# Optimization experiments

Hardware: AMD Instinct MI355X
Metric: run time of the kernel (lower is better)

The kernel has to match this reference:

```python
import jax, jax.numpy as jnp
import numpy as np

EPS = 1e-3  # Keras BatchNormalization default epsilon


def _conv2d_same(x, w):
    # x: [N,H,W,Cin], w: [kh,kw,Cin,Cout]
    return jax.lax.conv_general_dilated(
        x, w, window_strides=(1, 1), padding='SAME',
        dimension_numbers=('NHWC', 'HWIO', 'NHWC'))


def _hard_sigmoid(x):
    return jnp.clip(0.2 * x + 0.5, 0.0, 1.0)


def _convlstm2d(x, Wx, Wh, b):
    # x: [B,T,H,W,Cin]; Wx: [3,3,Cin,4F]; Wh: [3,3,F,4F]; b: [4F]
    B, T, H, W, Cin = x.shape
    F = Wh.shape[2]
    # precompute input-to-gate convs for all timesteps at once
    xg = _conv2d_same(x.reshape(B * T, H, W, Cin), Wx).reshape(B, T, H, W, 4 * F) + b

    def step(carry, xt):
        h, c = carry
        g = xt + _conv2d_same(h, Wh)
        gi, gf, gc, go = jnp.split(g, 4, axis=-1)  # Keras gate order i,f,c,o
        i = _hard_sigmoid(gi)
        f = _hard_sigmoid(gf)
        o = _hard_sigmoid(go)
        c = f * c + i * jnp.tanh(gc)
        h = o * jnp.tanh(c)
        return (h, c), h

    h0 = jnp.zeros((B, H, W, F), x.dtype)
    (_, _), hs = jax.lax.scan(step, (h0, h0), jnp.moveaxis(xg, 1, 0))
    return jnp.moveaxis(hs, 0, 1)  # [B,T,H,W,F]


def _batchnorm(x, g, be, m, v):
    # inference-mode BN over channel axis
    return (x - m) * (g * jax.lax.rsqrt(v + EPS)) + be


def setup_inputs() -> dict:
    key = jax.random.key(0)
    ks = jax.random.split(key, 10)
    B, T, H, W, C, F, NC = 16, 64, 16, 16, 6, 96, 10
    s = 0.05
    x = jax.random.normal(ks[0], (B, T, H, W, C), jnp.float32)
    Wx0 = jax.random.normal(ks[1], (3, 3, C, 4 * F), jnp.float32) * s
    Wh0 = jax.random.normal(ks[2], (3, 3, F, 4 * F), jnp.float32) * s
    b0 = jnp.zeros((4 * F,), jnp.float32)
    g0 = jnp.ones((F,), jnp.float32)
    be0 = jnp.zeros((F,), jnp.float32)
    m0 = jax.random.normal(ks[3], (F,), jnp.float32) * 0.1
    v0 = jax.random.uniform(ks[4], (F,), jnp.float32) + 0.5
    Wx1 = jax.random.normal(ks[5], (3, 3, F, 4 * F), jnp.float32) * s
    Wh1 = jax.random.normal(ks[6], (3, 3, F, 4 * F), jnp.float32) * s
    b1 = jnp.zeros((4 * F,), jnp.float32)
    g1 = jnp.ones((F,), jnp.float32)
    be1 = jnp.zeros((F,), jnp.float32)
    m1 = jax.random.normal(ks[7], (F,), jnp.float32) * 0.1
    v1 = jax.random.uniform(ks[8], (F,), jnp.float32) + 0.5
    Wd = jax.random.normal(ks[9], (T * H * W * F, NC), jnp.float32) * 0.001
    bd = jnp.zeros((NC,), jnp.float32)
    return dict(x=x, Wx0=Wx0, Wh0=Wh0, b0=b0, g0=g0, be0=be0, m0=m0, v0=v0,
                Wx1=Wx1, Wh1=Wh1, b1=b1, g1=g1, be1=be1, m1=m1, v1=v1,
                Wd=Wd, bd=bd)


def reference(x, Wx0, Wh0, b0, g0, be0, m0, v0,
              Wx1, Wh1, b1, g1, be1, m1, v1, Wd, bd):
    h = _convlstm2d(x, Wx0, Wh0, b0)
    h = _batchnorm(h, g0, be0, m0, v0)
    h = _convlstm2d(h, Wx1, Wh1, b1)
    h = _batchnorm(h, g1, be1, m1, v1)
    B = h.shape[0]
    flat = h.reshape(B, -1)  # Keras Flatten (row-major, channels-last)
    return flat @ Wd + bd
```

## Files before the change

kernel.cpp:

```cpp
#include <hip/hip_runtime.h>
#include <math.h>


typedef __attribute__((ext_vector_type(8))) short     bf16x8;
typedef __attribute__((ext_vector_type(8))) unsigned short u16x8;
typedef __attribute__((ext_vector_type(4))) float     f32x4;
typedef unsigned short u16;

#define RS 393216

__device__ __forceinline__ float hsig(float x) {
    return fminf(fmaxf(0.2f * x + 0.5f, 0.0f), 1.0f);
}
__device__ __forceinline__ float bf2f(u16 u) {
    union { unsigned int i; float f; } v; v.i = ((unsigned int)u) << 16; return v.f;
}
__device__ __forceinline__ u16 f2bf(float f) {
    union { float f; unsigned int i; } v; v.f = f;
    unsigned int r = (v.i + 0x7FFFu + ((v.i >> 16) & 1u)) >> 16;
    return (u16)r;
}

__device__ __forceinline__ void gridbar(unsigned* ctrs, unsigned* epoch,
                                        unsigned k, int blk)
{
    __syncthreads();
    if (threadIdx.x == 0) {
        __builtin_amdgcn_fence(__ATOMIC_RELEASE, "agent");
        __hip_atomic_fetch_add(ctrs + (blk & 63) * 64, 1u,
                               __ATOMIC_RELAXED, __HIP_MEMORY_SCOPE_AGENT);
    }
    if (blk == 0 && threadIdx.x < 64) {
        const unsigned target = k * 256u;
        unsigned sum;
        do {
            unsigned v = __hip_atomic_load(ctrs + threadIdx.x * 64,
                                           __ATOMIC_RELAXED,
                                           __HIP_MEMORY_SCOPE_AGENT);
            sum = v;
#pragma unroll
            for (int m = 1; m < 64; m <<= 1)
                sum += __shfl_xor(sum, m, 64);
            if (sum < target) __builtin_amdgcn_s_sleep(2);
        } while (sum < target);
        if (threadIdx.x == 0)
            __hip_atomic_store(epoch, k, __ATOMIC_RELAXED,
                               __HIP_MEMORY_SCOPE_AGENT);
    }
    if (threadIdx.x == 0) {
        while (__hip_atomic_load(epoch, __ATOMIC_RELAXED,
                                 __HIP_MEMORY_SCOPE_AGENT) < k)
            __builtin_amdgcn_s_sleep(4);
        __builtin_amdgcn_fence(__ATOMIC_ACQUIRE, "agent");
    }
    __syncthreads();
}

__device__ __forceinline__ void xbar(unsigned* slots, int myslot,
                                     unsigned target)
{
    __syncthreads();
    if (threadIdx.x == 0)
        __hip_atomic_fetch_add(slots + myslot * 32, 1u,
                               __ATOMIC_RELAXED, __HIP_MEMORY_SCOPE_AGENT);
    if (threadIdx.x < 32) {
        unsigned sum;
        do {
            unsigned v = __hip_atomic_load(slots + threadIdx.x * 32,
                                           __ATOMIC_RELAXED,
                                           __HIP_MEMORY_SCOPE_AGENT);
            sum = v;
#pragma unroll
            for (int m = 1; m < 32; m <<= 1)
                sum += __shfl_xor(sum, m, 64);
            if (sum < target) __builtin_amdgcn_s_sleep(2);
        } while (sum < target);
        asm volatile("buffer_inv sc0\n\ts_waitcnt vmcnt(0)" ::: "memory");
    }
    __syncthreads();
}

__global__ __launch_bounds__(256) void prep_x(const float* __restrict__ x,
                                              u16* __restrict__ xpad)
{
    const int idx = blockIdx.x * 256 + threadIdx.x;
    const int t = idx >> 12, b = (idx >> 8) & 15, p = idx & 255;
    const float* src = x + (((size_t)b * 64 + t) * 256 + p) * 6;
    u16x8 v = {};
    v[0] = f2bf(src[0]); v[1] = f2bf(src[1]); v[2] = f2bf(src[2]);
    v[3] = f2bf(src[3]); v[4] = f2bf(src[4]); v[5] = f2bf(src[5]);
    *(u16x8*)(xpad + (size_t)idx * 8) = v;
}

__global__ __launch_bounds__(256) void wtrans0(const float* __restrict__ Wx0,
                                               const float* __restrict__ Wh0,
                                               u16* __restrict__ Wt0)
{
    const int idx = blockIdx.x * 256 + threadIdx.x;
    const int n = idx / 960, k = idx - n * 960;
    const int nt = n / 96, j = n - nt * 96;
    const int no = (j / 24) * 96 + nt * 24 + (j % 24);
    float v = 0.0f;
    if (k < 96) {
        const int q = k >> 3, c = k & 7;
        if (q < 9 && c < 6) v = Wx0[(q * 6 + c) * 384 + no];
    } else {
        v = Wh0[(k - 96) * 384 + no];
    }
    Wt0[idx] = f2bf(v);
}

__global__ __launch_bounds__(256) void wtrans1(const float* __restrict__ Wx1,
                                               const float* __restrict__ Wh1,
                                               u16* __restrict__ Wt1)
{
    const int idx = blockIdx.x * 256 + threadIdx.x;
    const int n = idx / 1728, k = idx - n * 1728;
    const int nt = n / 96, j = n - nt * 96;
    const int no = (j / 24) * 96 + nt * 24 + (j % 24);
    const float v = (k < 864) ? Wx1[k * 384 + no] : Wh1[(k - 864) * 384 + no];
    Wt1[idx] = f2bf(v);
}

__global__ __launch_bounds__(256) void wtransD(const float* __restrict__ Wd,
                                               u16* __restrict__ WdT)
{
    const int k = blockIdx.x * 256 + threadIdx.x;
    const float* src = Wd + (size_t)k * 10;
#pragma unroll
    for (int nc = 0; nc < 10; ++nc)
        WdT[(size_t)nc * 1572864 + k] = f2bf(src[nc]);
}

__device__ void phase(int t, int m0, int n0, int tidx, char* lds,
    const u16* __restrict__ xpad, u16* __restrict__ h0b,
    u16* __restrict__ h1b, u16* __restrict__ h0bnb, u16* __restrict__ hall,
    const u16* __restrict__ Wt0, const u16* __restrict__ Wt1,
    const float* __restrict__ b0, const float* __restrict__ b1,
    const float* __restrict__ g0, const float* __restrict__ be0,
    const float* __restrict__ mu0, const float* __restrict__ v0,
    const float* __restrict__ g1, const float* __restrict__ be1,
    const float* __restrict__ mu1, const float* __restrict__ v1,
    float (&cregs)[6])
{
    const int half = tidx >> 8;
    const int htid = tidx & 255;
    const bool active = half ? (t < 63) : (t >= 0);

    const u16* in0 = half ? (xpad + (size_t)(t + 1) * 32768)
                          : (h0bnb + (size_t)(t & 1) * RS);
    const u16* in1 = half ? (h0b + (size_t)(t & 1) * RS)
                          : (h1b + (size_t)((t - 1) & 1) * RS);
    u16* hraw_out = half ? (h0b + (size_t)((t + 1) & 1) * RS)
                         : (h1b + (size_t)(t & 1) * RS);
    u16* hbn_out  = half ? (h0bnb + (size_t)((t + 1) & 1) * RS)
                         : (hall + (size_t)(t < 0 ? 0 : t) * RS);

    const int lane = htid & 63;
    const int hw   = htid >> 6;
    const int wm = hw >> 1, wn = hw & 1;
    const int fr = lane & 15, fg = lane >> 4;
    const int arow = htid >> 2, seg = htid & 3;
    const int mg = m0 + arow;
    const int py = (mg >> 4) & 15, px = mg & 15, pb = mg >> 8;
    const int nt = n0 / 96;

    const int   KT   = half ? 960 : 1728;
    const int   NS0  = half ? 3   : 27;
    const int   MYST = half ? 30  : 54;
    const u16*  Wt   = half ? Wt0 : Wt1;

    u16*   AsB  = (u16*)(lds + half * 25600);
    u16*   BsB  = AsB + 5120;
    float* accS = (float*)(lds + half * 25600);

    f32x4 acc[2][3];
#pragma unroll
    for (int i = 0; i < 2; ++i)
#pragma unroll
        for (int j = 0; j < 3; ++j) acc[i][j] = (f32x4){0.f, 0.f, 0.f, 0.f};

    u16x8 va, vb0, vb1;
    auto stage = [&](int ks) {
        u16x8 z = {};
        va = z;
        if (half && ks < 3) {
            const int q = ks * 4 + seg;
            const int qd = q / 3;
            const int yy = py + qd - 1;
            const int xx = px + (q - 3 * qd) - 1;
            if (q < 9 && (unsigned)yy < 16u && (unsigned)xx < 16u)
                va = *(const u16x8*)(in0 + (size_t)((pb << 8) + yy * 16 + xx) * 8);
        } else {
            const int s = (ks < NS0) ? ks : ks - NS0;
            const u16* src = (ks < NS0) ? in0 : in1;
            const int q = s / 3;
            const int c0v = (s - 3 * q) * 32 + seg * 8;
            const int qd = q / 3;
            const int yy = py + qd - 1;
            const int xx = px + (q - 3 * qd) - 1;
            if ((unsigned)yy < 16u && (unsigned)xx < 16u)
                va = *(const u16x8*)(src + (size_t)((pb << 8) + yy * 16 + xx) * 96 + c0v);
        }
        const int koff = ks * 32 + seg * 8;
        vb0 = *(const u16x8*)(Wt + (size_t)(n0 + arow) * KT + koff);
        vb1 = z;
        if (htid < 128)
            vb1 = *(const u16x8*)(Wt + (size_t)(n0 + 64 + arow) * KT + koff);
    };
    auto ldsw = [&](int buf) {
        *(u16x8*)(AsB + buf * 2560 + arow * 40 + seg * 8) = va;
        *(u16x8*)(BsB + buf * 3840 + arow * 40 + seg * 8) = vb0;
        if (htid < 128)
            *(u16x8*)(BsB + buf * 3840 + (64 + arow) * 40 + seg * 8) = vb1;
    };

    if (active) { stage(0); ldsw(0); }
    __syncthreads();

    for (int ks = 0; ks < 54; ++ks) {
        const int cur = ks & 1;
        if (active && ks < MYST) {
            if (ks + 1 < MYST) stage(ks + 1);

            bf16x8 af[2], bq[3];
#pragma unroll
            for (int mf = 0; mf < 2; ++mf)
                af[mf] = *(const bf16x8*)(AsB + cur * 2560 +
                                          (wm * 32 + mf * 16 + fr) * 40 + fg * 8);
#pragma unroll
            for (int nf = 0; nf < 3; ++nf)
                bq[nf] = *(const bf16x8*)(BsB + cur * 3840 +
                                          (wn * 48 + nf * 16 + fr) * 40 + fg * 8);

            __builtin_amdgcn_s_setprio(1);
#pragma unroll
            for (int mf = 0; mf < 2; ++mf)
#pragma unroll
                for (int nf = 0; nf < 3; ++nf)
                    acc[mf][nf] = __builtin_amdgcn_mfma_f32_16x16x32_bf16(
                        af[mf], bq[nf], acc[mf][nf], 0, 0, 0);
            __builtin_amdgcn_s_setprio(0);

            if (ks + 1 < MYST) ldsw(cur ^ 1);
        }
        __syncthreads();
    }

    if (active) {
        const float* bias = half ? b0 : b1;
#pragma unroll
        for (int nf = 0; nf < 3; ++nf) {
            const int col = wn * 48 + nf * 16 + fr;
            const float bi = bias[(col / 24) * 96 + nt * 24 + (col % 24)];
#pragma unroll
            for (int mf = 0; mf < 2; ++mf) {
                const int row = wm * 32 + mf * 16 + fg * 4;
#pragma unroll
                for (int r = 0; r < 4; ++r)
                    accS[(row + r) * 100 + col] = acc[mf][nf][r] + bi;
            }
        }
    }
    __syncthreads();

    if (active) {
        const float* gam = half ? g0 : g1;
        const float* bet = half ? be0 : be1;
        const float* muv = half ? mu0 : mu1;
        const float* var = half ? v0  : v1;
#pragma unroll
        for (int q = 0; q < 6; ++q) {
            const int item = htid + 256 * q;
            const int r = item / 24, fl = item - r * 24;
            const float gi = accS[r * 100 + fl];
            const float gf = accS[r * 100 + 24 + fl];
            const float gc = accS[r * 100 + 48 + fl];
            const float go = accS[r * 100 + 72 + fl];
            const int f = nt * 24 + fl;
            const float i_ = hsig(gi);
            const float f_ = hsig(gf);
            const float o_ = hsig(go);
            const float c_ = f_ * cregs[q] + i_ * tanhf(gc);
            const float h_ = o_ * tanhf(c_);
            cregs[q] = c_;
            hraw_out[(size_t)(m0 + r) * 96 + f] = f2bf(h_);
            const float s = gam[f] * rsqrtf(var[f] + 1e-3f);
            hbn_out[(size_t)(m0 + r) * 96 + f] =
                f2bf((h_ - muv[f]) * s + bet[f]);
        }
    }
}

__global__ __launch_bounds__(512, 2) void fused(
    unsigned* bctrs, unsigned* bepoch, unsigned* reg8, unsigned* xslots,
    const u16* xpad, u16* h0b, u16* h1b, u16* h0bnb, u16* hall,
    const u16* Wt0, const u16* Wt1,
    const float* b0, const float* b1,
    const float* g0, const float* be0, const float* mu0, const float* v0,
    const float* g1, const float* be1, const float* mu1, const float* v1)
{
    __shared__ char lds[51200];
    __shared__ unsigned shinfo[3];
    const int blk = blockIdx.x;

    if (threadIdx.x == 0) {
        unsigned xcc;
        asm volatile("s_getreg_b32 %0, hwreg(HW_REG_XCC_ID)" : "=s"(xcc));
        xcc &= 7u;
        unsigned slot = __hip_atomic_fetch_add(reg8 + xcc * 64, 1u,
                                               __ATOMIC_RELAXED,
                                               __HIP_MEMORY_SCOPE_AGENT);
        shinfo[0] = xcc; shinfo[1] = slot;
    }
    gridbar(bctrs, bepoch, 1, blk);
    if (threadIdx.x == 0) {
        unsigned ok = 1;
#pragma unroll
        for (int k = 0; k < 8; ++k)
            ok &= (__hip_atomic_load(reg8 + k * 64, __ATOMIC_RELAXED,
                                     __HIP_MEMORY_SCOPE_AGENT) == 32u);
        shinfo[2] = ok;
    }
    __syncthreads();
    const unsigned grp  = shinfo[0];
    const unsigned slot = shinfo[1];
    const bool grouped  = (shinfo[2] != 0u);

    float cregs[6] = {0.f, 0.f, 0.f, 0.f, 0.f, 0.f};

    if (grouped) {
        const int m0 = (int)grp * 512 + (int)(slot >> 2) * 64;
        const int n0 = (int)(slot & 3) * 96;
        unsigned* gs = xslots + grp * 1024;
        unsigned bar = 0;
        for (int t = -1; t < 64; ++t) {
            phase(t, m0, n0, threadIdx.x, lds, xpad, h0b, h1b, h0bnb, hall,
                  Wt0, Wt1, b0, b1, g0, be0, mu0, v0, g1, be1, mu1, v1, cregs);
            xbar(gs, (int)slot, (++bar) * 32u);
        }
    } else {
        const int m0 = (blk >> 2) * 64;
        const int n0 = (blk & 3) * 96;
        unsigned bar = 1;
        for (int t = -1; t < 64; ++t) {
            phase(t, m0, n0, threadIdx.x, lds, xpad, h0b, h1b, h0bnb, hall,
                  Wt0, Wt1, b0, b1, g0, be0, mu0, v0, g1, be1, mu1, v1, cregs);
            gridbar(bctrs, bepoch, ++bar, blk);
        }
    }
}

__global__ __launch_bounds__(512, 2) void stepF(int t,
    const u16* xpad, u16* h0b, u16* h1b, u16* h0bnb, u16* hall,
    const u16* Wt0, const u16* Wt1,
    const float* b0, const float* b1,
    const float* g0, const float* be0, const float* mu0, const float* v0,
    const float* g1, const float* be1, const float* mu1, const float* v1,
    float* c0g, float* c1g)
{
    __shared__ char lds[51200];
    const int m0 = (blockIdx.x >> 2) * 64;
    const int n0 = (blockIdx.x & 3) * 96;
    const int half = threadIdx.x >> 8;
    const int htid = threadIdx.x & 255;
    const int nt = n0 / 96;
    float* cst = half ? c0g : c1g;

    float cregs[6];
#pragma unroll
    for (int q = 0; q < 6; ++q) {
        const int item = htid + 256 * q;
        const int r = item / 24, fl = item - r * 24;
        cregs[q] = cst[(size_t)(m0 + r) * 96 + nt * 24 + fl];
    }
    phase(t, m0, n0, threadIdx.x, lds, xpad, h0b, h1b, h0bnb, hall,
          Wt0, Wt1, b0, b1, g0, be0, mu0, v0, g1, be1, mu1, v1, cregs);
#pragma unroll
    for (int q = 0; q < 6; ++q) {
        const int item = htid + 256 * q;
        const int r = item / 24, fl = item - r * 24;
        cst[(size_t)(m0 + r) * 96 + nt * 24 + fl] = cregs[q];
    }
}

__global__ void dense_partial(const u16* __restrict__ hall,
                              const u16* __restrict__ WdT,
                              float* __restrict__ partial)
{
    const int k0 = blockIdx.x * 2048;
    const int tt = k0 / 24576;
    const int r0 = k0 - tt * 24576;
    const int th = threadIdx.x;
    const int b  = th / 10;
    const int nc = th - b * 10;
    const u16* hp = hall + (size_t)(tt * 16 + b) * 24576 + r0;
    const u16* wp = WdT + (size_t)nc * 1572864 + k0;
    float acc = 0.0f;
    for (int j = 0; j < 2048; j += 8) {
        const u16x8 hv = *(const u16x8*)(hp + j);
        const u16x8 wv = *(const u16x8*)(wp + j);
#pragma unroll
        for (int u = 0; u < 8; ++u)
            acc = fmaf(bf2f(hv[u]), bf2f(wv[u]), acc);
    }
    partial[blockIdx.x * 160 + th] = acc;
}

__global__ void dense_reduce(const float* __restrict__ partial,
                             const float* __restrict__ bd,
                             float* __restrict__ out)
{
    const int t = threadIdx.x;
    const int nc = t - (t / 10) * 10;
    float acc = bd[nc];
    for (int p = 0; p < 768; ++p) acc += partial[p * 160 + t];
    out[t] = acc;
}

extern "C" void kernel_launch(void* const* d_in, const int* in_sizes, int n_in,
                              void* d_out, int out_size, void* d_ws, size_t ws_size,
                              hipStream_t stream)
{
    const float* x    = (const float*)d_in[0];
    const float* Wx0  = (const float*)d_in[1];
    const float* Wh0  = (const float*)d_in[2];
    const float* b0p  = (const float*)d_in[3];
    const float* g0p  = (const float*)d_in[4];
    const float* be0p = (const float*)d_in[5];
    const float* mu0p = (const float*)d_in[6];
    const float* v0p  = (const float*)d_in[7];
    const float* Wx1  = (const float*)d_in[8];
    const float* Wh1  = (const float*)d_in[9];
    const float* b1p  = (const float*)d_in[10];
    const float* g1p  = (const float*)d_in[11];
    const float* be1p = (const float*)d_in[12];
    const float* mu1p = (const float*)d_in[13];
    const float* v1p  = (const float*)d_in[14];
    const float* Wd   = (const float*)d_in[15];
    const float* bd   = (const float*)d_in[16];
    float* out = (float*)d_out;

    char* base = (char*)d_ws;
    u16*   h0b    = (u16*)(base);
    u16*   h1b    = (u16*)(base + 1572864);
    u16*   h0bnb  = (u16*)(base + 3145728);
    float* c0g    = (float*)(base + 4718592);
    float* c1g    = (float*)(base + 6291456);
    u16*   xpad   = (u16*)(base + 7864320);
    u16*   Wt0    = (u16*)(base + 12058624);
    u16*   Wt1    = (u16*)(base + 12795904);
    u16*   hall   = (u16*)(base + 14123008);
    float* part   = (float*)(base + 64454656);
    u16*   WdT    = (u16*)(base + 64946176);
    unsigned* bctrs  = (unsigned*)(base + 96403456);
    unsigned* bepoch = (unsigned*)(base + 96419840);
    unsigned* reg8   = (unsigned*)(base + 96420096);
    unsigned* xslots = (unsigned*)(base + 96422144);

    hipMemsetAsync(base, 0, 7864320, stream);
    hipMemsetAsync(bctrs, 0, 51456, stream);

    prep_x <<<1024, 256, 0, stream>>>(x, xpad);
    wtrans0<<<1440, 256, 0, stream>>>(Wx0, Wh0, Wt0);
    wtrans1<<<2592, 256, 0, stream>>>(Wx1, Wh1, Wt1);
    wtransD<<<6144, 256, 0, stream>>>(Wd, WdT);

    void* args[] = {
        (void*)&bctrs, (void*)&bepoch, (void*)&reg8, (void*)&xslots,
        (void*)&xpad, (void*)&h0b, (void*)&h1b, (void*)&h0bnb, (void*)&hall,
        (void*)&Wt0, (void*)&Wt1, (void*)&b0p, (void*)&b1p,
        (void*)&g0p, (void*)&be0p, (void*)&mu0p, (void*)&v0p,
        (void*)&g1p, (void*)&be1p, (void*)&mu1p, (void*)&v1p
    };
    hipError_t ce = hipLaunchCooperativeKernel((void*)fused, dim3(256),
                                               dim3(512), args, 0, stream);
    if (ce != hipSuccess) {
        (void)hipGetLastError();
        for (int t = -1; t < 64; ++t) {
            stepF<<<256, 512, 0, stream>>>(t, xpad, h0b, h1b, h0bnb, hall,
                                           Wt0, Wt1, b0p, b1p,
                                           g0p, be0p, mu0p, v0p,
                                           g1p, be1p, mu1p, v1p, c0g, c1g);
        }
    }

    dense_partial<<<768, 160, 0, stream>>>(hall, WdT, part);
    dense_reduce <<<1, 160, 0, stream>>>(part, bd, out);
}
```

Measured before the change: 1.975 ms.

## Load A fragments directly from global into registers, skipping LDS staging

The im2col A operand is now gathered straight from global memory into per-lane MFMA fragment registers, with two register sets (even/odd) prefetched two k-steps ahead, instead of being staged through LDS. Only the weight (B) tile still goes through double-buffered LDS, now with a row stride of 36 instead of 40. This removes the A-side LDS writes and reads and cuts LDS footprint. In exchange each lane issues scattered global loads, and duplicated A rows across waves are no longer shared, so global or cache traffic may rise.

```diff
diff --git a/kernel.cpp b/kernel.cpp
--- a/kernel.cpp
+++ b/kernel.cpp
@@ -19,6 +19,12 @@
     union { float f; unsigned int i; } v; v.f = f;
     unsigned int r = (v.i + 0x7FFFu + ((v.i >> 16) & 1u)) >> 16;
     return (u16)r;
+}
+__device__ __forceinline__ bf16x8 zsel(int4 v, bool ok) {
+    union { int4 i; bf16x8 b; } u;
+    u.i.x = ok ? v.x : 0; u.i.y = ok ? v.y : 0;
+    u.i.z = ok ? v.z : 0; u.i.w = ok ? v.w : 0;
+    return u.b;
 }
 
 __device__ __forceinline__ void gridbar(unsigned* ctrs, unsigned* epoch,
@@ -161,8 +167,7 @@
     const int wm = hw >> 1, wn = hw & 1;
     const int fr = lane & 15, fg = lane >> 4;
     const int arow = htid >> 2, seg = htid & 3;
-    const int mg = m0 + arow;
-    const int py = (mg >> 4) & 15, px = mg & 15, pb = mg >> 8;
+    const int pb = m0 >> 8;
     const int nt = n0 / 96;
 
     const int   KT   = half ? 960 : 1728;
@@ -170,8 +175,7 @@
     const int   MYST = half ? 30  : 54;
     const u16*  Wt   = half ? Wt0 : Wt1;
 
-    u16*   AsB  = (u16*)(lds + half * 25600);
-    u16*   BsB  = AsB + 5120;
+    u16*   BsB  = (u16*)(lds + half * 25600);
     float* accS = (float*)(lds + half * 25600);
 
     f32x4 acc[2][3];
@@ -180,70 +184,99 @@
 #pragma unroll
         for (int j = 0; j < 3; ++j) acc[i][j] = (f32x4){0.f, 0.f, 0.f, 0.f};
 
-    u16x8 va, vb0, vb1;
-    auto stage = [&](int ks) {
-        u16x8 z = {};
-        va = z;
-        if (half && ks < 3) {
-            const int q = ks * 4 + seg;
-            const int qd = q / 3;
-            const int yy = py + qd - 1;
-            const int xx = px + (q - 3 * qd) - 1;
-            if (q < 9 && (unsigned)yy < 16u && (unsigned)xx < 16u)
-                va = *(const u16x8*)(in0 + (size_t)((pb << 8) + yy * 16 + xx) * 8);
-        } else {
-            const int s = (ks < NS0) ? ks : ks - NS0;
-            const u16* src = (ks < NS0) ? in0 : in1;
-            const int q = s / 3;
-            const int c0v = (s - 3 * q) * 32 + seg * 8;
-            const int qd = q / 3;
-            const int yy = py + qd - 1;
-            const int xx = px + (q - 3 * qd) - 1;
-            if ((unsigned)yy < 16u && (unsigned)xx < 16u)
-                va = *(const u16x8*)(src + (size_t)((pb << 8) + yy * 16 + xx) * 96 + c0v);
+    int yf[2];
+#pragma unroll
+    for (int mf = 0; mf < 2; ++mf)
+        yf[mf] = ((m0 + wm * 32 + mf * 16) >> 4) & 15;
+
+    auto loadA = [&](int ks, bf16x8 (&af)[2]) {
+#pragma unroll
+        for (int mf = 0; mf < 2; ++mf) {
+            if (half && ks < 3) {
+                const int q  = ks * 4 + fg;
+                const int qd = q / 3;
+                const int qx = q - 3 * qd;
+                const int yy = yf[mf] + qd - 1;
+                const int xx = fr + qx - 1;
+                const bool ok = (q < 9) & ((unsigned)yy < 16u) &
+                                ((unsigned)xx < 16u);
+                const int yyc = yy < 0 ? 0 : (yy > 15 ? 15 : yy);
+                const int xxc = xx < 0 ? 0 : (xx > 15 ? 15 : xx);
+                const int4 v = *(const int4*)(in0 +
+                    (size_t)((pb << 8) + yyc * 16 + xxc) * 8);
+                af[mf] = zsel(v, ok);
+            } else {
+                const int s = (ks < NS0) ? ks : ks - NS0;
+                const u16* src = (ks < NS0) ? in0 : in1;
+                const int q  = s / 3;
+                const int c0 = (s - 3 * q) * 32 + fg * 8;
+                const int qd = q / 3;
+                const int qx = q - 3 * qd;
+                const int yy = yf[mf] + qd - 1;
+                if ((unsigned)yy < 16u) {
+                    const int xx = fr + qx - 1;
+                    const int xxc = xx < 0 ? 0 : (xx > 15 ? 15 : xx);
+                    const int4 v = *(const int4*)(src +
+                        (size_t)((pb << 8) + yy * 16 + xxc) * 96 + c0);
+                    af[mf] = zsel(v, (unsigned)xx < 16u);
+                } else {
+                    const bf16x8 z = {};
+                    af[mf] = z;
+                }
+            }
         }
+    };
+
+    u16x8 vb0, vb1;
+    auto stageB = [&](int ks) {
         const int koff = ks * 32 + seg * 8;
         vb0 = *(const u16x8*)(Wt + (size_t)(n0 + arow) * KT + koff);
-        vb1 = z;
         if (htid < 128)
             vb1 = *(const u16x8*)(Wt + (size_t)(n0 + 64 + arow) * KT + koff);
     };
-    auto ldsw = [&](int buf) {
-        *(u16x8*)(AsB + buf * 2560 + arow * 40 + seg * 8) = va;
-        *(u16x8*)(BsB + buf * 3840 + arow * 40 + seg * 8) = vb0;
+    auto writeB = [&](int buf) {
+        *(u16x8*)(BsB + buf * 3456 + arow * 36 + seg * 8) = vb0;
         if (htid < 128)
-            *(u16x8*)(BsB + buf * 3840 + (64 + arow) * 40 + seg * 8) = vb1;
+            *(u16x8*)(BsB + buf * 3456 + (64 + arow) * 36 + seg * 8) = vb1;
     };
 
-    if (active) { stage(0); ldsw(0); }
-    __syncthreads();
-
-    for (int ks = 0; ks < 54; ++ks) {
-        const int cur = ks & 1;
-        if (active && ks < MYST) {
-            if (ks + 1 < MYST) stage(ks + 1);
-
-            bf16x8 af[2], bq[3];
-#pragma unroll
-            for (int mf = 0; mf < 2; ++mf)
-                af[mf] = *(const bf16x8*)(AsB + cur * 2560 +
-                                          (wm * 32 + mf * 16 + fr) * 40 + fg * 8);
+    bf16x8 afe[2], afo[2];
+
+    if (active) {
+        loadA(0, afe);
+        loadA(1, afo);
+        stageB(0);
+        writeB(0);
+    }
+    __syncthreads();
+
+    auto step = [&](int ks, bf16x8 (&af)[2]) {
+        if (ks + 1 < MYST) stageB(ks + 1);
+
+        bf16x8 bq[3];
+#pragma unroll
+        for (int nf = 0; nf < 3; ++nf)
+            bq[nf] = *(const bf16x8*)(BsB + (ks & 1) * 3456 +
+                                      (wn * 48 + nf * 16 + fr) * 36 + fg * 8);
+
+        __builtin_amdgcn_s_setprio(1);
+#pragma unroll
+        for (int mf = 0; mf < 2; ++mf)
 #pragma unroll
             for (int nf = 0; nf < 3; ++nf)
-                bq[nf] = *(const bf16x8*)(BsB + cur * 3840 +
-                                          (wn * 48 + nf * 16 + fr) * 40 + fg * 8);
-
-            __builtin_amdgcn_s_setprio(1);
-#pragma unroll
-            for (int mf = 0; mf < 2; ++mf)
-#pragma unroll
-                for (int nf = 0; nf < 3; ++nf)
-                    acc[mf][nf] = __builtin_amdgcn_mfma_f32_16x16x32_bf16(
-                        af[mf], bq[nf], acc[mf][nf], 0, 0, 0);
-            __builtin_amdgcn_s_setprio(0);
-
-            if (ks + 1 < MYST) ldsw(cur ^ 1);
-        }
+                acc[mf][nf] = __builtin_amdgcn_mfma_f32_16x16x32_bf16(
+                    af[mf], bq[nf], acc[mf][nf], 0, 0, 0);
+        __builtin_amdgcn_s_setprio(0);
+
+        if (ks + 2 < MYST) loadA(ks + 2, af);
+        if (ks + 1 < MYST) writeB((ks + 1) & 1);
+    };
+
+    for (int ko = 0; ko < 27; ++ko) {
+        const int ks = ko * 2;
+        if (active && ks < MYST) step(ks, afe);
+        __syncthreads();
+        if (active && ks + 1 < MYST) step(ks + 1, afo);
         __syncthreads();
     }
 
```

Result: slower. 4.060 ms (+105.6%).
